# Optimization experiments

Measured on AMD Instinct MI355X. Metric: run time of the kernel, lower is better.

The kernel has to match this reference:

```python
import jax, jax.numpy as jnp
import numpy as np

N_NODES = 100000
N_EDGES = 1000000
IN_DIM = 128
HID1 = 64
HID2 = 64
OUT_DIM = 1
NUM_GRAPHS = 2048


def setup_inputs() -> dict:
    key = jax.random.key(0)
    ks = jax.random.split(key, 12)
    x = jax.random.normal(ks[0], (N_NODES, IN_DIM), dtype=jnp.float32)
    edge_index = jax.random.randint(ks[1], (2, N_EDGES), 0, N_NODES, dtype=jnp.int64)
    batch = jnp.sort(jax.random.randint(ks[2], (N_NODES,), 0, NUM_GRAPHS, dtype=jnp.int64))
    s1 = 1.0 / np.sqrt(IN_DIM)
    s2 = 1.0 / np.sqrt(HID1)
    s3 = 1.0 / np.sqrt(HID2)
    return {
        "x": x,
        "edge_index": edge_index,
        "batch": batch,
        "W1": jax.random.normal(ks[3], (IN_DIM, HID1), dtype=jnp.float32) * s1,
        "b1": jnp.zeros((HID1,), dtype=jnp.float32),
        "W2": jax.random.normal(ks[4], (HID1, HID2), dtype=jnp.float32) * s2,
        "b2": jnp.zeros((HID2,), dtype=jnp.float32),
        "attn_w": jax.random.normal(ks[5], (HID2, 1), dtype=jnp.float32) * s3,
        "attn_b": jnp.zeros((1,), dtype=jnp.float32),
        "mask_w": jax.random.normal(ks[6], (HID2, 1), dtype=jnp.float32) * s3,
        "mask_b": jnp.zeros((1,), dtype=jnp.float32),
        "out_w": jax.random.normal(ks[7], (HID2, OUT_DIM), dtype=jnp.float32) * s3,
        "out_b": jnp.zeros((OUT_DIM,), dtype=jnp.float32),
    }


def reference(x, edge_index, batch, W1, b1, W2, b2, attn_w, attn_b, mask_w, mask_b, out_w, out_b):
    n = x.shape[0]
    # GCNConv (PyG default): add self-loops, symmetric normalization
    loop = jnp.arange(n, dtype=edge_index.dtype)
    row = jnp.concatenate([edge_index[0], loop])  # source nodes
    col = jnp.concatenate([edge_index[1], loop])  # target nodes
    deg = jax.ops.segment_sum(jnp.ones_like(col, dtype=x.dtype), col, num_segments=n)
    dinv = jnp.where(deg > 0, jax.lax.rsqrt(jnp.maximum(deg, 1e-12)), 0.0)
    norm = dinv[row] * dinv[col]  # [E+N]

    def conv(h, W, b):
        h = h @ W                              # [N, out]
        m = h[row] * norm[:, None]             # gather + scale  [E+N, out]
        return jax.ops.segment_sum(m, col, num_segments=n) + b

    h = jax.nn.relu(conv(x, W1, b1))
    h = jax.nn.relu(conv(h, W2, b2))
    # AttentionPooling: (attn score * sigmoid mask)-weighted scatter-sum per graph
    scores = (h @ attn_w + attn_b) * jax.nn.sigmoid(h @ mask_w + mask_b)  # [N,1]
    pooled = jax.ops.segment_sum(h * scores, batch, num_segments=NUM_GRAPHS)  # [G, HID2]
    return pooled @ out_w + out_b
```

## Files before the change

kernel.cpp:

```cpp
#include <hip/hip_runtime.h>
#include <math.h>


#define NB 64
#define SEG 16
#define CAPS 80
#define SLOTS (SEG * CAPS)
#define BIN_BLOCKS 256

__global__ __launch_bounds__(256) void gemm_bin_kernel(
    const float* __restrict__ X, const float* __restrict__ W,
    float* __restrict__ P, int N, int K,
    const int* __restrict__ row, const int* __restrict__ col,
    int* __restrict__ bcnt, int* __restrict__ gbuf, int E,
    float* __restrict__ out, const float* __restrict__ out_b, int G) {
    __shared__ float Wl[32 * 64];
    __shared__ float xs[128 * 33];

    if (blockIdx.x < BIN_BLOCKS) {
        int seg = blockIdx.x & (SEG - 1);
        int t = blockIdx.x * 256 + threadIdx.x;
        if (t < G) out[t] = out_b[0];
        for (int e = t; e < E; e += BIN_BLOCKS * 256) {
            int c = col[e];
            int b = c >> 6;
            int pos = atomicAdd(&bcnt[(b * SEG + seg) * 16], 1);
            if (pos < CAPS) gbuf[b * SLOTS + seg * CAPS + pos] = row[e] | ((c & 63) << 17);
        }
        return;
    }

    const int tid = threadIdx.x;
    const int cg = tid & 3;
    const int ng = tid >> 2;
    const int node0 = (blockIdx.x - BIN_BLOCKS) * 128;

    float acc[2][16];
#pragma unroll
    for (int r = 0; r < 2; r++)
#pragma unroll
        for (int j = 0; j < 16; j++) acc[r][j] = 0.0f;

    for (int k0 = 0; k0 < K; k0 += 32) {
        const float4* Wg = (const float4*)(W + (size_t)k0 * 64);
#pragma unroll
        for (int f = tid; f < 512; f += 256) ((float4*)Wl)[f] = Wg[f];
        {
            int rrow = tid >> 1;
            int q0 = (tid & 1) * 16;
            int node = node0 + rrow;
            const float* Xr = X + (size_t)node * K + k0 + q0;
            float* xd = &xs[rrow * 33 + q0];
#pragma unroll
            for (int q = 0; q < 4; q++) {
                float4 v = make_float4(0.f, 0.f, 0.f, 0.f);
                if (node < N) v = *(const float4*)(Xr + 4 * q);
                xd[4 * q + 0] = v.x;
                xd[4 * q + 1] = v.y;
                xd[4 * q + 2] = v.z;
                xd[4 * q + 3] = v.w;
            }
        }
        __syncthreads();
#pragma unroll
        for (int kk = 0; kk < 32; kk++) {
            float xv0 = xs[(ng * 2 + 0) * 33 + kk];
            float xv1 = xs[(ng * 2 + 1) * 33 + kk];
            const float* wr = &Wl[kk * 64 + cg * 4];
            float4 w0 = *(const float4*)(wr + 0);
            float4 w1 = *(const float4*)(wr + 16);
            float4 w2 = *(const float4*)(wr + 32);
            float4 w3 = *(const float4*)(wr + 48);
#pragma unroll
            for (int r = 0; r < 2; r++) {
                float xv = r ? xv1 : xv0;
                acc[r][0]  = fmaf(xv, w0.x, acc[r][0]);
                acc[r][1]  = fmaf(xv, w0.y, acc[r][1]);
                acc[r][2]  = fmaf(xv, w0.z, acc[r][2]);
                acc[r][3]  = fmaf(xv, w0.w, acc[r][3]);
                acc[r][4]  = fmaf(xv, w1.x, acc[r][4]);
                acc[r][5]  = fmaf(xv, w1.y, acc[r][5]);
                acc[r][6]  = fmaf(xv, w1.z, acc[r][6]);
                acc[r][7]  = fmaf(xv, w1.w, acc[r][7]);
                acc[r][8]  = fmaf(xv, w2.x, acc[r][8]);
                acc[r][9]  = fmaf(xv, w2.y, acc[r][9]);
                acc[r][10] = fmaf(xv, w2.z, acc[r][10]);
                acc[r][11] = fmaf(xv, w2.w, acc[r][11]);
                acc[r][12] = fmaf(xv, w3.x, acc[r][12]);
                acc[r][13] = fmaf(xv, w3.y, acc[r][13]);
                acc[r][14] = fmaf(xv, w3.z, acc[r][14]);
                acc[r][15] = fmaf(xv, w3.w, acc[r][15]);
            }
        }
        __syncthreads();
    }

#pragma unroll
    for (int r = 0; r < 2; r++) {
        int node = node0 + ng * 2 + r;
        if (node < N) {
            float* dst = P + (size_t)node * 64 + cg * 4;
#pragma unroll
            for (int m = 0; m < 4; m++) {
                float4 v = make_float4(acc[r][4 * m + 0], acc[r][4 * m + 1],
                                       acc[r][4 * m + 2], acc[r][4 * m + 3]);
                *(float4*)(dst + 16 * m) = v;
            }
        }
    }
}

__global__ __launch_bounds__(256) void sort_kernel(
    const int* __restrict__ bcnt, const int* __restrict__ gbuf,
    int* __restrict__ csr, int* __restrict__ startcnt,
    float* __restrict__ dinv, int N) {
    __shared__ int scnt[SEG], segoff[SEG], s_tot;
    __shared__ int ebuf[SLOTS];
    __shared__ int lcnt[NB], lcur[NB];
    const int tid = threadIdx.x;
    const int b = blockIdx.x;
    const int base = b * SLOTS;

    if (tid < SEG) {
        int c = bcnt[(b * SEG + tid) * 16];
        scnt[tid] = c < CAPS ? c : CAPS;
    }
    if (tid < NB) lcnt[tid] = 0;
    __syncthreads();
    if (tid == 0) {
        int o = 0;
        for (int s = 0; s < SEG; s++) { segoff[s] = o; o += scnt[s]; }
        s_tot = o;
    }
    __syncthreads();
    for (int idx = tid; idx < SLOTS; idx += 256) {
        int seg = idx / CAPS;
        int j = idx - seg * CAPS;
        if (j < scnt[seg]) {
            int w = gbuf[base + idx];
            ebuf[segoff[seg] + j] = w;
            atomicAdd(&lcnt[(w >> 17) & 63], 1);
        }
    }
    __syncthreads();
    if (tid < NB) {
        int cntv = lcnt[tid];
        int rnd = (cntv + 3) & ~3;
        int val = rnd;
#pragma unroll
        for (int off = 1; off < 64; off <<= 1) {
            int n = __shfl_up(val, off, 64);
            if (tid >= off) val += n;
        }
        int st = val - rnd;
        lcur[tid] = st;
        int v = b * NB + tid;
        if (v < N) {
            dinv[v] = rsqrtf(1.0f + (float)cntv);
            int cc = cntv < 127 ? cntv : 127;
            startcnt[v] = ((base + st) << 7) | cc;
        }
    }
    __syncthreads();
    int tot = s_tot;
    for (int idx = tid; idx < tot; idx += 256) {
        int w = ebuf[idx];
        int vl = (w >> 17) & 63;
        int pp = atomicAdd(&lcur[vl], 1);
        csr[base + pp] = w & 131071;
    }
}

__global__ __launch_bounds__(256) void gather_kernel(
    const float* __restrict__ P, const int* __restrict__ csr,
    const int* __restrict__ startcnt, const float* __restrict__ dinv,
    const float* __restrict__ bias, float* __restrict__ B, int N) {
    int t = blockIdx.x * blockDim.x + threadIdx.x;
    int v = t >> 4;
    if (v >= N) return;
    int p4 = (t & 15) * 4;
    int pack = startcnt[v];
    int st = pack >> 7;
    int c = pack & 127;
    float dv = dinv[v];
    float4 a0 = *(const float4*)(P + (size_t)v * 64 + p4);
    float4 acc = make_float4(a0.x * dv, a0.y * dv, a0.z * dv, a0.w * dv);
    for (int i = 0; i < c; i += 8) {
        int4 ua = *(const int4*)(csr + st + i);
        int4 ub = *(const int4*)(csr + st + i + 4);
        float du0 = dinv[ua.x], du1 = dinv[ua.y], du2 = dinv[ua.z], du3 = dinv[ua.w];
        float du4 = dinv[ub.x], du5 = dinv[ub.y], du6 = dinv[ub.z], du7 = dinv[ub.w];
        float4 m0 = *(const float4*)(P + (size_t)ua.x * 64 + p4);
        float4 m1 = *(const float4*)(P + (size_t)ua.y * 64 + p4);
        float4 m2 = *(const float4*)(P + (size_t)ua.z * 64 + p4);
        float4 m3 = *(const float4*)(P + (size_t)ua.w * 64 + p4);
        float4 m4 = *(const float4*)(P + (size_t)ub.x * 64 + p4);
        float4 m5 = *(const float4*)(P + (size_t)ub.y * 64 + p4);
        float4 m6 = *(const float4*)(P + (size_t)ub.z * 64 + p4);
        float4 m7 = *(const float4*)(P + (size_t)ub.w * 64 + p4);
        acc.x = fmaf(m0.x, du0, acc.x); acc.y = fmaf(m0.y, du0, acc.y);
        acc.z = fmaf(m0.z, du0, acc.z); acc.w = fmaf(m0.w, du0, acc.w);
        if (i + 1 < c) { acc.x = fmaf(m1.x, du1, acc.x); acc.y = fmaf(m1.y, du1, acc.y);
                         acc.z = fmaf(m1.z, du1, acc.z); acc.w = fmaf(m1.w, du1, acc.w); }
        if (i + 2 < c) { acc.x = fmaf(m2.x, du2, acc.x); acc.y = fmaf(m2.y, du2, acc.y);
                         acc.z = fmaf(m2.z, du2, acc.z); acc.w = fmaf(m2.w, du2, acc.w); }
        if (i + 3 < c) { acc.x = fmaf(m3.x, du3, acc.x); acc.y = fmaf(m3.y, du3, acc.y);
                         acc.z = fmaf(m3.z, du3, acc.z); acc.w = fmaf(m3.w, du3, acc.w); }
        if (i + 4 < c) { acc.x = fmaf(m4.x, du4, acc.x); acc.y = fmaf(m4.y, du4, acc.y);
                         acc.z = fmaf(m4.z, du4, acc.z); acc.w = fmaf(m4.w, du4, acc.w); }
        if (i + 5 < c) { acc.x = fmaf(m5.x, du5, acc.x); acc.y = fmaf(m5.y, du5, acc.y);
                         acc.z = fmaf(m5.z, du5, acc.z); acc.w = fmaf(m5.w, du5, acc.w); }
        if (i + 6 < c) { acc.x = fmaf(m6.x, du6, acc.x); acc.y = fmaf(m6.y, du6, acc.y);
                         acc.z = fmaf(m6.z, du6, acc.z); acc.w = fmaf(m6.w, du6, acc.w); }
        if (i + 7 < c) { acc.x = fmaf(m7.x, du7, acc.x); acc.y = fmaf(m7.y, du7, acc.y);
                         acc.z = fmaf(m7.z, du7, acc.z); acc.w = fmaf(m7.w, du7, acc.w); }
    }
    float4 bb = *(const float4*)(bias + p4);
    float4 r;
    r.x = fmaxf(fmaf(acc.x, dv, bb.x), 0.f);
    r.y = fmaxf(fmaf(acc.y, dv, bb.y), 0.f);
    r.z = fmaxf(fmaf(acc.z, dv, bb.z), 0.f);
    r.w = fmaxf(fmaf(acc.w, dv, bb.w), 0.f);
    *(float4*)(B + (size_t)v * 64 + p4) = r;
}

__global__ __launch_bounds__(256) void gemm_scale_kernel(
    const float* __restrict__ X, const float* __restrict__ W,
    const float* __restrict__ dinv, float* __restrict__ Q, int N, int K) {
    __shared__ float Wl[32 * 64];
    __shared__ float xs[128 * 33];
    const int tid = threadIdx.x;
    const int cg = tid & 3;
    const int ng = tid >> 2;
    const int node0 = blockIdx.x * 128;

    float acc[2][16];
#pragma unroll
    for (int r = 0; r < 2; r++)
#pragma unroll
        for (int j = 0; j < 16; j++) acc[r][j] = 0.0f;

    for (int k0 = 0; k0 < K; k0 += 32) {
        const float4* Wg = (const float4*)(W + (size_t)k0 * 64);
#pragma unroll
        for (int f = tid; f < 512; f += 256) ((float4*)Wl)[f] = Wg[f];
        {
            int rrow = tid >> 1;
            int q0 = (tid & 1) * 16;
            int node = node0 + rrow;
            const float* Xr = X + (size_t)node * K + k0 + q0;
            float* xd = &xs[rrow * 33 + q0];
#pragma unroll
            for (int q = 0; q < 4; q++) {
                float4 v = make_float4(0.f, 0.f, 0.f, 0.f);
                if (node < N) v = *(const float4*)(Xr + 4 * q);
                xd[4 * q + 0] = v.x;
                xd[4 * q + 1] = v.y;
                xd[4 * q + 2] = v.z;
                xd[4 * q + 3] = v.w;
            }
        }
        __syncthreads();
#pragma unroll
        for (int kk = 0; kk < 32; kk++) {
            float xv0 = xs[(ng * 2 + 0) * 33 + kk];
            float xv1 = xs[(ng * 2 + 1) * 33 + kk];
            const float* wr = &Wl[kk * 64 + cg * 4];
            float4 w0 = *(const float4*)(wr + 0);
            float4 w1 = *(const float4*)(wr + 16);
            float4 w2 = *(const float4*)(wr + 32);
            float4 w3 = *(const float4*)(wr + 48);
#pragma unroll
            for (int r = 0; r < 2; r++) {
                float xv = r ? xv1 : xv0;
                acc[r][0]  = fmaf(xv, w0.x, acc[r][0]);
                acc[r][1]  = fmaf(xv, w0.y, acc[r][1]);
                acc[r][2]  = fmaf(xv, w0.z, acc[r][2]);
                acc[r][3]  = fmaf(xv, w0.w, acc[r][3]);
                acc[r][4]  = fmaf(xv, w1.x, acc[r][4]);
                acc[r][5]  = fmaf(xv, w1.y, acc[r][5]);
                acc[r][6]  = fmaf(xv, w1.z, acc[r][6]);
                acc[r][7]  = fmaf(xv, w1.w, acc[r][7]);
                acc[r][8]  = fmaf(xv, w2.x, acc[r][8]);
                acc[r][9]  = fmaf(xv, w2.y, acc[r][9]);
                acc[r][10] = fmaf(xv, w2.z, acc[r][10]);
                acc[r][11] = fmaf(xv, w2.w, acc[r][11]);
                acc[r][12] = fmaf(xv, w3.x, acc[r][12]);
                acc[r][13] = fmaf(xv, w3.y, acc[r][13]);
                acc[r][14] = fmaf(xv, w3.z, acc[r][14]);
                acc[r][15] = fmaf(xv, w3.w, acc[r][15]);
            }
        }
        __syncthreads();
    }

#pragma unroll
    for (int r = 0; r < 2; r++) {
        int node = node0 + ng * 2 + r;
        if (node < N) {
            float d = dinv[node];
            float* dst = Q + (size_t)node * 64 + cg * 4;
#pragma unroll
            for (int m = 0; m < 4; m++) {
                float4 v = make_float4(acc[r][4 * m + 0] * d, acc[r][4 * m + 1] * d,
                                       acc[r][4 * m + 2] * d, acc[r][4 * m + 3] * d);
                *(float4*)(dst + 16 * m) = v;
            }
        }
    }
}

#define GP_NODES 64
__global__ __launch_bounds__(256) void gather_pool_kernel(
    const float* __restrict__ Q, const int* __restrict__ csr,
    const int* __restrict__ startcnt, const float* __restrict__ dinv,
    const float* __restrict__ bias, const int* __restrict__ batch,
    const float* __restrict__ attn_w, const float* __restrict__ attn_b,
    const float* __restrict__ mask_w, const float* __restrict__ mask_b,
    const float* __restrict__ out_w, float* __restrict__ out, int N) {
    __shared__ float pacc[2048];
    __shared__ int s_gmin, s_span;
    const int tid = threadIdx.x;
    const int v0 = blockIdx.x * GP_NODES;
    const int vend = (v0 + GP_NODES < N) ? v0 + GP_NODES : N;
    if (tid == 0) {
        int gmin = batch[v0];
        s_gmin = gmin;
        s_span = batch[vend - 1] - gmin + 1;
    }
    __syncthreads();
    const int gmin = s_gmin, span = s_span;
    for (int i = tid; i < span; i += 256) pacc[i] = 0.f;
    __syncthreads();

    const int p = tid & 15;
    const int p4 = p * 4;
    const float4 wa = ((const float4*)attn_w)[p];
    const float4 wm = ((const float4*)mask_w)[p];
    const float4 wo = ((const float4*)out_w)[p];
    const float4 bb = ((const float4*)bias)[p];
    const float ab = attn_b[0], mb = mask_b[0];

    for (int v = v0 + (tid >> 4); v < vend; v += 16) {
        int pack = startcnt[v];
        int st = pack >> 7;
        int c = pack & 127;
        float dv = dinv[v];
        float4 acc = *(const float4*)(Q + (size_t)v * 64 + p4);
        for (int i = 0; i < c; i += 8) {
            int4 ua = *(const int4*)(csr + st + i);
            int4 ub = *(const int4*)(csr + st + i + 4);
            float4 m0 = *(const float4*)(Q + (size_t)ua.x * 64 + p4);
            float4 m1 = *(const float4*)(Q + (size_t)ua.y * 64 + p4);
            float4 m2 = *(const float4*)(Q + (size_t)ua.z * 64 + p4);
            float4 m3 = *(const float4*)(Q + (size_t)ua.w * 64 + p4);
            float4 m4 = *(const float4*)(Q + (size_t)ub.x * 64 + p4);
            float4 m5 = *(const float4*)(Q + (size_t)ub.y * 64 + p4);
            float4 m6 = *(const float4*)(Q + (size_t)ub.z * 64 + p4);
            float4 m7 = *(const float4*)(Q + (size_t)ub.w * 64 + p4);
            acc.x += m0.x; acc.y += m0.y; acc.z += m0.z; acc.w += m0.w;
            if (i + 1 < c) { acc.x += m1.x; acc.y += m1.y; acc.z += m1.z; acc.w += m1.w; }
            if (i + 2 < c) { acc.x += m2.x; acc.y += m2.y; acc.z += m2.z; acc.w += m2.w; }
            if (i + 3 < c) { acc.x += m3.x; acc.y += m3.y; acc.z += m3.z; acc.w += m3.w; }
            if (i + 4 < c) { acc.x += m4.x; acc.y += m4.y; acc.z += m4.z; acc.w += m4.w; }
            if (i + 5 < c) { acc.x += m5.x; acc.y += m5.y; acc.z += m5.z; acc.w += m5.w; }
            if (i + 6 < c) { acc.x += m6.x; acc.y += m6.y; acc.z += m6.z; acc.w += m6.w; }
            if (i + 7 < c) { acc.x += m7.x; acc.y += m7.y; acc.z += m7.z; acc.w += m7.w; }
        }
        float hx = fmaxf(fmaf(acc.x, dv, bb.x), 0.f);
        float hy = fmaxf(fmaf(acc.y, dv, bb.y), 0.f);
        float hz = fmaxf(fmaf(acc.z, dv, bb.z), 0.f);
        float hw = fmaxf(fmaf(acc.w, dv, bb.w), 0.f);
        float pa = hx * wa.x + hy * wa.y + hz * wa.z + hw * wa.w;
        float pm = hx * wm.x + hy * wm.y + hz * wm.z + hw * wm.w;
        float po = hx * wo.x + hy * wo.y + hz * wo.z + hw * wo.w;
#pragma unroll
        for (int off = 1; off < 16; off <<= 1) {
            pa += __shfl_xor(pa, off, 64);
            pm += __shfl_xor(pm, off, 64);
            po += __shfl_xor(po, off, 64);
        }
        if (p == 0) {
            float cc = (pa + ab) * (1.0f / (1.0f + expf(-(pm + mb)))) * po;
            atomicAdd(&pacc[batch[v] - gmin], cc);
        }
    }
    __syncthreads();
    for (int i = tid; i < span; i += 256) {
        float val = pacc[i];
        if (val != 0.f) atomicAdd(&out[gmin + i], val);
    }
}

extern "C" void kernel_launch(void* const* d_in, const int* in_sizes, int n_in,
                              void* d_out, int out_size, void* d_ws, size_t ws_size,
                              hipStream_t stream) {
    const float* x      = (const float*)d_in[0];
    const int*   edge   = (const int*)d_in[1];
    const int*   batch  = (const int*)d_in[2];
    const float* W1     = (const float*)d_in[3];
    const float* b1     = (const float*)d_in[4];
    const float* W2     = (const float*)d_in[5];
    const float* b2     = (const float*)d_in[6];
    const float* attn_w = (const float*)d_in[7];
    const float* attn_b = (const float*)d_in[8];
    const float* mask_w = (const float*)d_in[9];
    const float* mask_b = (const float*)d_in[10];
    const float* out_w  = (const float*)d_in[11];
    const float* out_b  = (const float*)d_in[12];
    float* out = (float*)d_out;

    const int N  = in_sizes[2];
    const int E  = in_sizes[1] / 2;
    const int K1 = in_sizes[0] / N;
    const int H  = in_sizes[4];
    const int G  = out_size;
    const int* row = edge;
    const int* col = edge + E;

    const int NBUCK = (N + NB - 1) / NB;

    char* ws = (char*)d_ws;
    auto align256 = [](size_t s) { return (s + 255) / 256 * 256; };
    int*   bcnt     = (int*)ws;   ws += align256((size_t)NBUCK * SEG * 16 * 4);
    int*   gbuf     = (int*)ws;   ws += align256((size_t)NBUCK * SLOTS * 4);
    int*   csr      = (int*)ws;   ws += align256((size_t)NBUCK * SLOTS * 4);
    int*   startcnt = (int*)ws;   ws += align256((size_t)N * 4);
    float* dinv     = (float*)ws; ws += align256((size_t)N * 4);
    float* P        = (float*)ws; ws += align256((size_t)N * H * 4);
    float* B        = (float*)ws; ws += align256((size_t)N * H * 4);
    float* Q        = (float*)ws;

    const int gblocks = (N + 127) / 128;
    const int n16b = (N * 16 + 255) / 256;

    hipMemsetAsync(bcnt, 0, (size_t)NBUCK * SEG * 16 * 4, stream);
    hipMemsetAsync(csr, 0, (size_t)NBUCK * SLOTS * 4, stream);

    gemm_bin_kernel<<<BIN_BLOCKS + gblocks, 256, 0, stream>>>(
        x, W1, P, N, K1, row, col, bcnt, gbuf, E, out, out_b, G);

    sort_kernel<<<NBUCK, 256, 0, stream>>>(bcnt, gbuf, csr, startcnt, dinv, N);

    gather_kernel<<<n16b, 256, 0, stream>>>(P, csr, startcnt, dinv, b1, B, N);

    gemm_scale_kernel<<<gblocks, 256, 0, stream>>>(B, W2, dinv, Q, N, H);

    gather_pool_kernel<<<NBUCK, 256, 0, stream>>>(
        Q, csr, startcnt, dinv, b2, batch, attn_w, attn_b, mask_w, mask_b, out_w, out, N);
}
```

Baseline: 282.0 us.

## Fuse layer-1 gather with layer-2 GEMM via shared-memory hidden tile

Merges the first-layer neighbor gather/ReLU and the second-layer dense GEMM into one kernel: each block gathers 64 nodes into a shared-memory tile, then multiplies by W2 held in shared memory and writes the dinv-scaled result. This removes the intermediate B buffer's global write and read plus one kernel launch. In exchange, each block now loads all of W2 (16KB), uses about 33KB of shared memory, and each thread computes only one node row in the GEMM, which may reduce occupancy and GEMM efficiency.

```diff
diff --git a/kernel.cpp b/kernel.cpp
--- a/kernel.cpp
+++ b/kernel.cpp
@@ -171,141 +171,105 @@
     }
 }
 
-__global__ __launch_bounds__(256) void gather_kernel(
+__global__ __launch_bounds__(256) void gather_gemm_kernel(
     const float* __restrict__ P, const int* __restrict__ csr,
     const int* __restrict__ startcnt, const float* __restrict__ dinv,
-    const float* __restrict__ bias, float* __restrict__ B, int N) {
-    int t = blockIdx.x * blockDim.x + threadIdx.x;
-    int v = t >> 4;
-    if (v >= N) return;
-    int p4 = (t & 15) * 4;
-    int pack = startcnt[v];
-    int st = pack >> 7;
-    int c = pack & 127;
-    float dv = dinv[v];
-    float4 a0 = *(const float4*)(P + (size_t)v * 64 + p4);
-    float4 acc = make_float4(a0.x * dv, a0.y * dv, a0.z * dv, a0.w * dv);
-    for (int i = 0; i < c; i += 8) {
-        int4 ua = *(const int4*)(csr + st + i);
-        int4 ub = *(const int4*)(csr + st + i + 4);
-        float du0 = dinv[ua.x], du1 = dinv[ua.y], du2 = dinv[ua.z], du3 = dinv[ua.w];
-        float du4 = dinv[ub.x], du5 = dinv[ub.y], du6 = dinv[ub.z], du7 = dinv[ub.w];
-        float4 m0 = *(const float4*)(P + (size_t)ua.x * 64 + p4);
-        float4 m1 = *(const float4*)(P + (size_t)ua.y * 64 + p4);
-        float4 m2 = *(const float4*)(P + (size_t)ua.z * 64 + p4);
-        float4 m3 = *(const float4*)(P + (size_t)ua.w * 64 + p4);
-        float4 m4 = *(const float4*)(P + (size_t)ub.x * 64 + p4);
-        float4 m5 = *(const float4*)(P + (size_t)ub.y * 64 + p4);
-        float4 m6 = *(const float4*)(P + (size_t)ub.z * 64 + p4);
-        float4 m7 = *(const float4*)(P + (size_t)ub.w * 64 + p4);
-        acc.x = fmaf(m0.x, du0, acc.x); acc.y = fmaf(m0.y, du0, acc.y);
-        acc.z = fmaf(m0.z, du0, acc.z); acc.w = fmaf(m0.w, du0, acc.w);
-        if (i + 1 < c) { acc.x = fmaf(m1.x, du1, acc.x); acc.y = fmaf(m1.y, du1, acc.y);
-                         acc.z = fmaf(m1.z, du1, acc.z); acc.w = fmaf(m1.w, du1, acc.w); }
-        if (i + 2 < c) { acc.x = fmaf(m2.x, du2, acc.x); acc.y = fmaf(m2.y, du2, acc.y);
-                         acc.z = fmaf(m2.z, du2, acc.z); acc.w = fmaf(m2.w, du2, acc.w); }
-        if (i + 3 < c) { acc.x = fmaf(m3.x, du3, acc.x); acc.y = fmaf(m3.y, du3, acc.y);
-                         acc.z = fmaf(m3.z, du3, acc.z); acc.w = fmaf(m3.w, du3, acc.w); }
-        if (i + 4 < c) { acc.x = fmaf(m4.x, du4, acc.x); acc.y = fmaf(m4.y, du4, acc.y);
-                         acc.z = fmaf(m4.z, du4, acc.z); acc.w = fmaf(m4.w, du4, acc.w); }
-        if (i + 5 < c) { acc.x = fmaf(m5.x, du5, acc.x); acc.y = fmaf(m5.y, du5, acc.y);
-                         acc.z = fmaf(m5.z, du5, acc.z); acc.w = fmaf(m5.w, du5, acc.w); }
-        if (i + 6 < c) { acc.x = fmaf(m6.x, du6, acc.x); acc.y = fmaf(m6.y, du6, acc.y);
-                         acc.z = fmaf(m6.z, du6, acc.z); acc.w = fmaf(m6.w, du6, acc.w); }
-        if (i + 7 < c) { acc.x = fmaf(m7.x, du7, acc.x); acc.y = fmaf(m7.y, du7, acc.y);
-                         acc.z = fmaf(m7.z, du7, acc.z); acc.w = fmaf(m7.w, du7, acc.w); }
-    }
-    float4 bb = *(const float4*)(bias + p4);
-    float4 r;
-    r.x = fmaxf(fmaf(acc.x, dv, bb.x), 0.f);
-    r.y = fmaxf(fmaf(acc.y, dv, bb.y), 0.f);
-    r.z = fmaxf(fmaf(acc.z, dv, bb.z), 0.f);
-    r.w = fmaxf(fmaf(acc.w, dv, bb.w), 0.f);
-    *(float4*)(B + (size_t)v * 64 + p4) = r;
-}
-
-__global__ __launch_bounds__(256) void gemm_scale_kernel(
-    const float* __restrict__ X, const float* __restrict__ W,
-    const float* __restrict__ dinv, float* __restrict__ Q, int N, int K) {
-    __shared__ float Wl[32 * 64];
-    __shared__ float xs[128 * 33];
+    const float* __restrict__ b1, const float* __restrict__ W2,
+    float* __restrict__ Q, int N) {
+    __shared__ float hs[64 * 65];
+    __shared__ float Wl[64 * 64];
     const int tid = threadIdx.x;
+    const int v0 = blockIdx.x * 64;
+    const int vend = (v0 + 64 < N) ? v0 + 64 : N;
+    const int p = tid & 15;
+    const int p4 = p * 4;
+
+    for (int f = tid; f < 1024; f += 256)
+        ((float4*)Wl)[f] = ((const float4*)W2)[f];
+
+    const float4 bb = ((const float4*)b1)[p];
+    for (int v = v0 + (tid >> 4); v < vend; v += 16) {
+        int pack = startcnt[v];
+        int st = pack >> 7;
+        int c = pack & 127;
+        float dv = dinv[v];
+        float4 a0 = *(const float4*)(P + (size_t)v * 64 + p4);
+        float4 acc = make_float4(a0.x * dv, a0.y * dv, a0.z * dv, a0.w * dv);
+        for (int i = 0; i < c; i += 8) {
+            int4 ua = *(const int4*)(csr + st + i);
+            int4 ub = *(const int4*)(csr + st + i + 4);
+            float du0 = dinv[ua.x], du1 = dinv[ua.y], du2 = dinv[ua.z], du3 = dinv[ua.w];
+            float du4 = dinv[ub.x], du5 = dinv[ub.y], du6 = dinv[ub.z], du7 = dinv[ub.w];
+            float4 m0 = *(const float4*)(P + (size_t)ua.x * 64 + p4);
+            float4 m1 = *(const float4*)(P + (size_t)ua.y * 64 + p4);
+            float4 m2 = *(const float4*)(P + (size_t)ua.z * 64 + p4);
+            float4 m3 = *(const float4*)(P + (size_t)ua.w * 64 + p4);
+            float4 m4 = *(const float4*)(P + (size_t)ub.x * 64 + p4);
+            float4 m5 = *(const float4*)(P + (size_t)ub.y * 64 + p4);
+            float4 m6 = *(const float4*)(P + (size_t)ub.z * 64 + p4);
+            float4 m7 = *(const float4*)(P + (size_t)ub.w * 64 + p4);
+            acc.x = fmaf(m0.x, du0, acc.x); acc.y = fmaf(m0.y, du0, acc.y);
+            acc.z = fmaf(m0.z, du0, acc.z); acc.w = fmaf(m0.w, du0, acc.w);
+            if (i + 1 < c) { acc.x = fmaf(m1.x, du1, acc.x); acc.y = fmaf(m1.y, du1, acc.y);
+                             acc.z = fmaf(m1.z, du1, acc.z); acc.w = fmaf(m1.w, du1, acc.w); }
+            if (i + 2 < c) { acc.x = fmaf(m2.x, du2, acc.x); acc.y = fmaf(m2.y, du2, acc.y);
+                             acc.z = fmaf(m2.z, du2, acc.z); acc.w = fmaf(m2.w, du2, acc.w); }
+            if (i + 3 < c) { acc.x = fmaf(m3.x, du3, acc.x); acc.y = fmaf(m3.y, du3, acc.y);
+                             acc.z = fmaf(m3.z, du3, acc.z); acc.w = fmaf(m3.w, du3, acc.w); }
+            if (i + 4 < c) { acc.x = fmaf(m4.x, du4, acc.x); acc.y = fmaf(m4.y, du4, acc.y);
+                             acc.z = fmaf(m4.z, du4, acc.z); acc.w = fmaf(m4.w, du4, acc.w); }
+            if (i + 5 < c) { acc.x = fmaf(m5.x, du5, acc.x); acc.y = fmaf(m5.y, du5, acc.y);
+                             acc.z = fmaf(m5.z, du5, acc.z); acc.w = fmaf(m5.w, du5, acc.w); }
+            if (i + 6 < c) { acc.x = fmaf(m6.x, du6, acc.x); acc.y = fmaf(m6.y, du6, acc.y);
+                             acc.z = fmaf(m6.z, du6, acc.z); acc.w = fmaf(m6.w, du6, acc.w); }
+            if (i + 7 < c) { acc.x = fmaf(m7.x, du7, acc.x); acc.y = fmaf(m7.y, du7, acc.y);
+                             acc.z = fmaf(m7.z, du7, acc.z); acc.w = fmaf(m7.w, du7, acc.w); }
+        }
+        float* hd = &hs[(v - v0) * 65 + p4];
+        hd[0] = fmaxf(fmaf(acc.x, dv, bb.x), 0.f);
+        hd[1] = fmaxf(fmaf(acc.y, dv, bb.y), 0.f);
+        hd[2] = fmaxf(fmaf(acc.z, dv, bb.z), 0.f);
+        hd[3] = fmaxf(fmaf(acc.w, dv, bb.w), 0.f);
+    }
+    __syncthreads();
+
     const int cg = tid & 3;
-    const int ng = tid >> 2;
-    const int node0 = blockIdx.x * 128;
-
-    float acc[2][16];
-#pragma unroll
-    for (int r = 0; r < 2; r++)
-#pragma unroll
-        for (int j = 0; j < 16; j++) acc[r][j] = 0.0f;
-
-    for (int k0 = 0; k0 < K; k0 += 32) {
-        const float4* Wg = (const float4*)(W + (size_t)k0 * 64);
-#pragma unroll
-        for (int f = tid; f < 512; f += 256) ((float4*)Wl)[f] = Wg[f];
-        {
-            int rrow = tid >> 1;
-            int q0 = (tid & 1) * 16;
-            int node = node0 + rrow;
-            const float* Xr = X + (size_t)node * K + k0 + q0;
-            float* xd = &xs[rrow * 33 + q0];
-#pragma unroll
-            for (int q = 0; q < 4; q++) {
-                float4 v = make_float4(0.f, 0.f, 0.f, 0.f);
-                if (node < N) v = *(const float4*)(Xr + 4 * q);
-                xd[4 * q + 0] = v.x;
-                xd[4 * q + 1] = v.y;
-                xd[4 * q + 2] = v.z;
-                xd[4 * q + 3] = v.w;
-            }
-        }
-        __syncthreads();
-#pragma unroll
-        for (int kk = 0; kk < 32; kk++) {
-            float xv0 = xs[(ng * 2 + 0) * 33 + kk];
-            float xv1 = xs[(ng * 2 + 1) * 33 + kk];
-            const float* wr = &Wl[kk * 64 + cg * 4];
-            float4 w0 = *(const float4*)(wr + 0);
-            float4 w1 = *(const float4*)(wr + 16);
-            float4 w2 = *(const float4*)(wr + 32);
-            float4 w3 = *(const float4*)(wr + 48);
-#pragma unroll
-            for (int r = 0; r < 2; r++) {
-                float xv = r ? xv1 : xv0;
-                acc[r][0]  = fmaf(xv, w0.x, acc[r][0]);
-                acc[r][1]  = fmaf(xv, w0.y, acc[r][1]);
-                acc[r][2]  = fmaf(xv, w0.z, acc[r][2]);
-                acc[r][3]  = fmaf(xv, w0.w, acc[r][3]);
-                acc[r][4]  = fmaf(xv, w1.x, acc[r][4]);
-                acc[r][5]  = fmaf(xv, w1.y, acc[r][5]);
-                acc[r][6]  = fmaf(xv, w1.z, acc[r][6]);
-                acc[r][7]  = fmaf(xv, w1.w, acc[r][7]);
-                acc[r][8]  = fmaf(xv, w2.x, acc[r][8]);
-                acc[r][9]  = fmaf(xv, w2.y, acc[r][9]);
-                acc[r][10] = fmaf(xv, w2.z, acc[r][10]);
-                acc[r][11] = fmaf(xv, w2.w, acc[r][11]);
-                acc[r][12] = fmaf(xv, w3.x, acc[r][12]);
-                acc[r][13] = fmaf(xv, w3.y, acc[r][13]);
-                acc[r][14] = fmaf(xv, w3.z, acc[r][14]);
-                acc[r][15] = fmaf(xv, w3.w, acc[r][15]);
-            }
-        }
-        __syncthreads();
-    }
-
-#pragma unroll
-    for (int r = 0; r < 2; r++) {
-        int node = node0 + ng * 2 + r;
-        if (node < N) {
-            float d = dinv[node];
-            float* dst = Q + (size_t)node * 64 + cg * 4;
-#pragma unroll
-            for (int m = 0; m < 4; m++) {
-                float4 v = make_float4(acc[r][4 * m + 0] * d, acc[r][4 * m + 1] * d,
-                                       acc[r][4 * m + 2] * d, acc[r][4 * m + 3] * d);
-                *(float4*)(dst + 16 * m) = v;
-            }
+    const int n0 = tid >> 2;
+    float acc[16];
+#pragma unroll
+    for (int j = 0; j < 16; j++) acc[j] = 0.0f;
+    for (int kk = 0; kk < 64; kk++) {
+        float xv = hs[n0 * 65 + kk];
+        const float* wr = &Wl[kk * 64 + cg * 4];
+        float4 w0 = *(const float4*)(wr + 0);
+        float4 w1 = *(const float4*)(wr + 16);
+        float4 w2 = *(const float4*)(wr + 32);
+        float4 w3 = *(const float4*)(wr + 48);
+        acc[0]  = fmaf(xv, w0.x, acc[0]);
+        acc[1]  = fmaf(xv, w0.y, acc[1]);
+        acc[2]  = fmaf(xv, w0.z, acc[2]);
+        acc[3]  = fmaf(xv, w0.w, acc[3]);
+        acc[4]  = fmaf(xv, w1.x, acc[4]);
+        acc[5]  = fmaf(xv, w1.y, acc[5]);
+        acc[6]  = fmaf(xv, w1.z, acc[6]);
+        acc[7]  = fmaf(xv, w1.w, acc[7]);
+        acc[8]  = fmaf(xv, w2.x, acc[8]);
+        acc[9]  = fmaf(xv, w2.y, acc[9]);
+        acc[10] = fmaf(xv, w2.z, acc[10]);
+        acc[11] = fmaf(xv, w2.w, acc[11]);
+        acc[12] = fmaf(xv, w3.x, acc[12]);
+        acc[13] = fmaf(xv, w3.y, acc[13]);
+        acc[14] = fmaf(xv, w3.z, acc[14]);
+        acc[15] = fmaf(xv, w3.w, acc[15]);
+    }
+    int node = v0 + n0;
+    if (node < N) {
+        float d = dinv[node];
+        float* dst = Q + (size_t)node * 64 + cg * 4;
+        for (int m = 0; m < 4; m++) {
+            float4 v = make_float4(acc[4 * m + 0] * d, acc[4 * m + 1] * d,
+                                   acc[4 * m + 2] * d, acc[4 * m + 3] * d);
+            *(float4*)(dst + 16 * m) = v;
         }
     }
 }
@@ -428,11 +392,9 @@
     int*   startcnt = (int*)ws;   ws += align256((size_t)N * 4);
     float* dinv     = (float*)ws; ws += align256((size_t)N * 4);
     float* P        = (float*)ws; ws += align256((size_t)N * H * 4);
-    float* B        = (float*)ws; ws += align256((size_t)N * H * 4);
     float* Q        = (float*)ws;
 
     const int gblocks = (N + 127) / 128;
-    const int n16b = (N * 16 + 255) / 256;
 
     hipMemsetAsync(bcnt, 0, (size_t)NBUCK * SEG * 16 * 4, stream);
     hipMemsetAsync(csr, 0, (size_t)NBUCK * SLOTS * 4, stream);
@@ -442,9 +404,8 @@
 
     sort_kernel<<<NBUCK, 256, 0, stream>>>(bcnt, gbuf, csr, startcnt, dinv, N);
 
-    gather_kernel<<<n16b, 256, 0, stream>>>(P, csr, startcnt, dinv, b1, B, N);
-
-    gemm_scale_kernel<<<gblocks, 256, 0, stream>>>(B, W2, dinv, Q, N, H);
+    gather_gemm_kernel<<<NBUCK, 256, 0, stream>>>(
+        P, csr, startcnt, dinv, b1, W2, Q, N);
 
     gather_pool_kernel<<<NBUCK, 256, 0, stream>>>(
         Q, csr, startcnt, dinv, b2, batch, attn_w, attn_b, mask_w, mask_b, out_w, out, N);
```

Result: faster. 275.9 us (-2.2%).
